# Kernel optimization log

Hardware: AMD Instinct MI355X
Metric: run time of the kernel (lower is better)

Reference implementation:

```python
import jax, jax.numpy as jnp
import numpy as np

K = 3          # kernel size
DIL = 1        # dilation
PAD = (K + (K - 1) * (DIL - 1)) // 2   # = 1
CENTER = (K * K - 1) // 2              # = 4
D_MIN = 0.0
D_MAX = 10.0
MIN_NGHBR = 4


def _unfold(x):
    """x: (B,C,H,W) -> patches (B,H,W,k*k,C), matching torch.nn.Unfold ordering."""
    b, c, h, w = x.shape
    xp = jnp.pad(x, ((0, 0), (0, 0), (PAD, PAD), (PAD, PAD)))
    # fixed k*k=9 taps: loop over the kernel window only (not data dims)
    pats = [xp[:, :, i * DIL:i * DIL + h, j * DIL:j * DIL + w]
            for i in range(K) for j in range(K)]
    p = jnp.stack(pats, axis=2)          # (B,C,kk,H,W)
    return p.transpose(0, 3, 4, 2, 1)    # (B,H,W,kk,C)


def setup_inputs() -> dict:
    key = jax.random.key(0)
    kxy, kz = jax.random.split(key)
    B, H, W = 4, 480, 640
    xy = jax.random.normal(kxy, (B, 2, H, W), dtype=jnp.float32)
    z = jax.random.uniform(kz, (B, 1, H, W), dtype=jnp.float32, minval=0.1, maxval=9.9)
    points = jnp.concatenate([xy, z], axis=1)  # (B,3,H,W)
    return {"points": points}


def reference(points):
    b, _, h, w = points.shape
    # 3x3 neighborhoods of 3D points: (B,H,W,9,3)
    A3 = _unfold(points)
    # depth-validity mask, unfolded over the same window: (B,H,W,9,1)
    depth = points[:, 2:3]
    valid = ((depth > D_MIN) & (depth < D_MAX)).astype(points.dtype)
    vc = _unfold(valid)
    # homogeneous design matrix A = [x y z 1], zeroed where neighbor invalid
    A = jnp.concatenate([A3, jnp.ones_like(A3[..., :1])], axis=-1)  # (B,H,W,9,4)
    A = jnp.where(vc > 0.5, A, jnp.zeros_like(A))
    # normal equations: per-pixel symmetric PSD 4x4
    AtA = jnp.einsum('bhwki,bhwkj->bhwij', A, A)
    # A^T A is symmetric PSD -> real eigensystem; eigh gives ascending eigvals,
    # so the null-space direction (smallest eigval) is column 0.
    eig_val, eig_vec = jnp.linalg.eigh(AtA)
    normal4 = eig_vec[..., :, 0]                      # (B,H,W,4)
    normal = normal4[..., :3].transpose(0, 3, 1, 2)   # (B,3,H,W)
    # F.normalize(p=2, dim=1, eps=1e-12)
    nrm = jnp.linalg.norm(normal, axis=1, keepdims=True)
    normal = normal / jnp.maximum(nrm, 1e-12)
    # orient toward the camera ray
    flip = jnp.sign(jnp.sum(normal * points, axis=1, keepdims=True))
    normal = normal * flip
    # validity masks
    vm1 = vc[:, :, :, CENTER, 0][:, None] > 0.5                 # center pixel valid
    vm2 = jnp.sum(vc[..., 0], axis=3)[:, None] >= MIN_NGHBR    # enough neighbors
    # vm3 (real eigensystem) is always True for the symmetric solve
    vm4 = jnp.linalg.norm(normal, axis=1, keepdims=True) > 0.5
    valid_mask = vm1 & vm2 & vm4
    return normal, valid_mask
```

## Files before the change

### kernel.cpp

```cpp
#include <hip/hip_runtime.h>

#define BB 4
#define HH 480
#define WW 640

__device__ __forceinline__ double det3d(double a, double b, double c,
                                        double d, double e, double f,
                                        double g, double h, double i) {
    return a * (e * i - f * h) - b * (d * i - f * g) + c * (d * h - e * g);
}

__global__ __launch_bounds__(256) void d2n_kernel(const float* __restrict__ pts,
                                                  float* __restrict__ out) {
    int idx = blockIdx.x * 256 + threadIdx.x;
    if (idx >= BB * HH * WW) return;
    int x = idx % WW;
    int t1 = idx / WW;
    int y = t1 % HH;
    int b = t1 / HH;

    const size_t HW = (size_t)HH * WW;
    const float* xs = pts + ((size_t)b * 3 + 0) * HW;
    const float* ys = pts + ((size_t)b * 3 + 1) * HW;
    const float* zs = pts + ((size_t)b * 3 + 2) * HW;

    float px[9], py[9], pz[9];
    bool inb[9];
#pragma unroll
    for (int i = 0; i < 9; ++i) {
        int dy = i / 3 - 1, dx = i % 3 - 1;
        int yy = y + dy, xx = x + dx;
        inb[i] = ((unsigned)yy < HH) & ((unsigned)xx < WW);
        int yyc = min(max(yy, 0), HH - 1);
        int xxc = min(max(xx, 0), WW - 1);
        int o = yyc * WW + xxc;
        pz[i] = zs[o];
        px[i] = xs[o];
        py[i] = ys[o];
    }

    float sxx = 0.f, sxy = 0.f, sxz = 0.f, sx = 0.f;
    float syy = 0.f, syz = 0.f, sy = 0.f;
    float szz = 0.f, sz = 0.f, cnt = 0.f;
#pragma unroll
    for (int i = 0; i < 9; ++i) {
        float w = (inb[i] && pz[i] > 0.0f && pz[i] < 10.0f) ? 1.0f : 0.0f;
        float qx = px[i] * w, qy = py[i] * w, qz = pz[i] * w;
        sxx += qx * px[i]; sxy += qx * py[i]; sxz += qx * pz[i]; sx += qx;
        syy += qy * py[i]; syz += qy * pz[i]; sy += qy;
        szz += qz * pz[i]; sz += qz;
        cnt += w;
    }

    double tr = (double)sxx + (double)syy + (double)szz + (double)cnt;
    double it = 1.0 / tr;
    double m00 = sxx * it, m01 = sxy * it, m02 = sxz * it, m03 = sx * it;
    double m11 = syy * it, m12 = syz * it, m13 = sy * it;
    double m22 = szz * it, m23 = sz * it, m33 = cnt * it;

    double e1 = m00 + m11 + m22 + m33;
    double e2 = (m00 * m11 - m01 * m01) + (m00 * m22 - m02 * m02) +
                (m00 * m33 - m03 * m03) + (m11 * m22 - m12 * m12) +
                (m11 * m33 - m13 * m13) + (m22 * m33 - m23 * m23);
    double P0 = det3d(m11, m12, m13, m12, m22, m23, m13, m23, m33);
    double P1 = det3d(m00, m02, m03, m02, m22, m23, m03, m23, m33);
    double P2 = det3d(m00, m01, m03, m01, m11, m13, m03, m13, m33);
    double P3 = det3d(m00, m01, m02, m01, m11, m12, m02, m12, m22);
    double e3 = P0 + P1 + P2 + P3;
    double e4 = m00 * P0
              - m01 * det3d(m01, m12, m13, m02, m22, m23, m03, m23, m33)
              + m02 * det3d(m01, m11, m13, m02, m12, m23, m03, m13, m33)
              - m03 * det3d(m01, m11, m12, m02, m12, m22, m03, m13, m23);

    double lam = 0.0;
#pragma unroll
    for (int itn = 0; itn < 16; ++itn) {
        double p  = (((lam - e1) * lam + e2) * lam - e3) * lam + e4;
        double dp = ((4.0 * lam - 3.0 * e1) * lam + 2.0 * e2) * lam - e3;
        dp = fmin(dp, -1e-300);
        lam = lam - p / dp;
        lam = fmin(fmax(lam, 0.0), 0.26);
    }

    double d0 = m00 - lam, d1 = m11 - lam, d2 = m22 - lam, d3 = m33 - lam;
    double C00 =  det3d(d1, m12, m13, m12, d2, m23, m13, m23, d3);
    double C01 = -det3d(m01, m12, m13, m02, d2, m23, m03, m23, d3);
    double C02 =  det3d(m01, d1, m13, m02, m12, m23, m03, m13, d3);
    double C03 = -det3d(m01, d1, m12, m02, m12, d2, m03, m13, m23);
    double C11 =  det3d(d0, m02, m03, m02, d2, m23, m03, m23, d3);
    double C12 = -det3d(d0, m01, m03, m02, m12, m23, m03, m13, d3);
    double C13 =  det3d(d0, m01, m02, m02, m12, d2, m03, m13, m23);
    double C22 =  det3d(d0, m01, m03, m01, d1, m13, m03, m13, d3);
    double C23 = -det3d(d0, m01, m02, m01, d1, m12, m03, m13, m23);
    double C33 =  det3d(d0, m01, m02, m01, d1, m12, m02, m12, d2);

    double best = fabs(C00);
    double vx = C00, vy = C01, vz = C02;
    double a1 = fabs(C11);
    if (a1 > best) { best = a1; vx = C01; vy = C11; vz = C12; }
    double a2 = fabs(C22);
    if (a2 > best) { best = a2; vx = C02; vy = C12; vz = C22; }
    double a3 = fabs(C33);
    if (a3 > best) { best = a3; vx = C03; vy = C13; vz = C23; }

    double nd = vx * vx + vy * vy + vz * vz;
    double inv = 1.0 / fmax(sqrt(nd), 1e-300);
    float nx = (float)(vx * inv), ny = (float)(vy * inv), nz = (float)(vz * inv);

    int o = y * WW + x;
    float cx = px[4], cy = py[4], cz = pz[4];
    float dot = nx * cx + ny * cy + nz * cz;
    float sgn = (dot > 0.0f) ? 1.0f : ((dot < 0.0f) ? -1.0f : 0.0f);
    nx *= sgn; ny *= sgn; nz *= sgn;

    out[((size_t)b * 3 + 0) * HW + o] = nx;
    out[((size_t)b * 3 + 1) * HW + o] = ny;
    out[((size_t)b * 3 + 2) * HW + o] = nz;

    bool cvalid = (cz > 0.0f && cz < 10.0f);
    bool m = cvalid && (cnt >= 4.0f) && (nx * nx + ny * ny + nz * nz > 0.25f);
    out[(size_t)BB * 3 * HW + (size_t)b * HW + o] = m ? 1.0f : 0.0f;
}

extern "C" void kernel_launch(void* const* d_in, const int* in_sizes, int n_in,
                              void* d_out, int out_size, void* d_ws, size_t ws_size,
                              hipStream_t stream) {
    const float* pts = (const float*)d_in[0];
    float* out = (float*)d_out;
    int total = BB * HH * WW;
    d2n_kernel<<<(total + 255) / 256, 256, 0, stream>>>(pts, out);
}
```

Before: 93.57 us.

## Cut fp64 cost: symmetric determinants, fast reciprocals, fewer Newton iterations

Replaces the fp64 divisions with a float hardware reciprocal refined by one Newton step, and uses a cheaper symmetric 3x3 determinant form for the principal minors and diagonal cofactors. It also trims the Newton eigenvalue iterations from 16 to 14, hoists the clamped row and column indices, and moves the final normalization to float using rsq after scaling by the chosen diagonal cofactor. The aim is to cut fp64 division and sqrt throughput costs, which dominate this compute-bound kernel. The risks are lower precision from the approximate reciprocal, fewer iterations, and overflow or zero handling in frcp(vd), all of which could change results in degenerate cases.

```diff
diff --git a/kernel.cpp b/kernel.cpp
--- a/kernel.cpp
+++ b/kernel.cpp
@@ -8,6 +8,18 @@
                                         double d, double e, double f,
                                         double g, double h, double i) {
     return a * (e * i - f * h) - b * (d * i - f * g) + c * (d * h - e * g);
+}
+
+__device__ __forceinline__ double sdet3d(double a, double b, double c,
+                                         double e, double f, double i) {
+    return a * (e * i - f * f) + b * (2.0 * c * f - b * i) - c * c * e;
+}
+
+__device__ __forceinline__ double frcp(double d) {
+    float rf = __builtin_amdgcn_rcpf((float)d);
+    double r = (double)rf;
+    r = r * __builtin_fma(-d, r, 2.0);
+    return r;
 }
 
 __global__ __launch_bounds__(256) void d2n_kernel(const float* __restrict__ pts,
@@ -24,16 +36,23 @@
     const float* ys = pts + ((size_t)b * 3 + 1) * HW;
     const float* zs = pts + ((size_t)b * 3 + 2) * HW;
 
+    int row[3], col[3];
+    bool rin[3], cin[3];
+#pragma unroll
+    for (int k = 0; k < 3; ++k) {
+        int yy = y + k - 1, xx = x + k - 1;
+        rin[k] = (unsigned)yy < HH;
+        cin[k] = (unsigned)xx < WW;
+        row[k] = min(max(yy, 0), HH - 1) * WW;
+        col[k] = min(max(xx, 0), WW - 1);
+    }
     float px[9], py[9], pz[9];
     bool inb[9];
 #pragma unroll
     for (int i = 0; i < 9; ++i) {
-        int dy = i / 3 - 1, dx = i % 3 - 1;
-        int yy = y + dy, xx = x + dx;
-        inb[i] = ((unsigned)yy < HH) & ((unsigned)xx < WW);
-        int yyc = min(max(yy, 0), HH - 1);
-        int xxc = min(max(xx, 0), WW - 1);
-        int o = yyc * WW + xxc;
+        int r = i / 3, c = i % 3;
+        int o = row[r] + col[c];
+        inb[i] = rin[r] & cin[c];
         pz[i] = zs[o];
         px[i] = xs[o];
         py[i] = ys[o];
@@ -53,7 +72,7 @@
     }
 
     double tr = (double)sxx + (double)syy + (double)szz + (double)cnt;
-    double it = 1.0 / tr;
+    double it = frcp(tr);
     double m00 = sxx * it, m01 = sxy * it, m02 = sxz * it, m03 = sx * it;
     double m11 = syy * it, m12 = syz * it, m13 = sy * it;
     double m22 = szz * it, m23 = sz * it, m33 = cnt * it;
@@ -62,50 +81,54 @@
     double e2 = (m00 * m11 - m01 * m01) + (m00 * m22 - m02 * m02) +
                 (m00 * m33 - m03 * m03) + (m11 * m22 - m12 * m12) +
                 (m11 * m33 - m13 * m13) + (m22 * m33 - m23 * m23);
-    double P0 = det3d(m11, m12, m13, m12, m22, m23, m13, m23, m33);
-    double P1 = det3d(m00, m02, m03, m02, m22, m23, m03, m23, m33);
-    double P2 = det3d(m00, m01, m03, m01, m11, m13, m03, m13, m33);
-    double P3 = det3d(m00, m01, m02, m01, m11, m12, m02, m12, m22);
+    double P0 = sdet3d(m11, m12, m13, m22, m23, m33);
+    double P1 = sdet3d(m00, m02, m03, m22, m23, m33);
+    double P2 = sdet3d(m00, m01, m03, m11, m13, m33);
+    double P3 = sdet3d(m00, m01, m02, m11, m12, m22);
     double e3 = P0 + P1 + P2 + P3;
     double e4 = m00 * P0
               - m01 * det3d(m01, m12, m13, m02, m22, m23, m03, m23, m33)
               + m02 * det3d(m01, m11, m13, m02, m12, m23, m03, m13, m33)
               - m03 * det3d(m01, m11, m12, m02, m12, m22, m03, m13, m23);
 
+    double t31 = 3.0 * e1, t22 = 2.0 * e2;
     double lam = 0.0;
 #pragma unroll
-    for (int itn = 0; itn < 16; ++itn) {
+    for (int itn = 0; itn < 14; ++itn) {
         double p  = (((lam - e1) * lam + e2) * lam - e3) * lam + e4;
-        double dp = ((4.0 * lam - 3.0 * e1) * lam + 2.0 * e2) * lam - e3;
-        dp = fmin(dp, -1e-300);
-        lam = lam - p / dp;
+        double dp = ((4.0 * lam - t31) * lam + t22) * lam - e3;
+        dp = fmin(dp, -1e-30);
+        lam = lam - p * frcp(dp);
         lam = fmin(fmax(lam, 0.0), 0.26);
     }
 
     double d0 = m00 - lam, d1 = m11 - lam, d2 = m22 - lam, d3 = m33 - lam;
-    double C00 =  det3d(d1, m12, m13, m12, d2, m23, m13, m23, d3);
+    double C00 =  sdet3d(d1, m12, m13, d2, m23, d3);
+    double C11 =  sdet3d(d0, m02, m03, d2, m23, d3);
+    double C22 =  sdet3d(d0, m01, m03, d1, m13, d3);
+    double C33 =  sdet3d(d0, m01, m02, d1, m12, d2);
     double C01 = -det3d(m01, m12, m13, m02, d2, m23, m03, m23, d3);
     double C02 =  det3d(m01, d1, m13, m02, m12, m23, m03, m13, d3);
     double C03 = -det3d(m01, d1, m12, m02, m12, d2, m03, m13, m23);
-    double C11 =  det3d(d0, m02, m03, m02, d2, m23, m03, m23, d3);
     double C12 = -det3d(d0, m01, m03, m02, m12, m23, m03, m13, d3);
     double C13 =  det3d(d0, m01, m02, m02, m12, d2, m03, m13, m23);
-    double C22 =  det3d(d0, m01, m03, m01, d1, m13, m03, m13, d3);
     double C23 = -det3d(d0, m01, m02, m01, d1, m12, m03, m13, m23);
-    double C33 =  det3d(d0, m01, m02, m01, d1, m12, m02, m12, d2);
 
     double best = fabs(C00);
-    double vx = C00, vy = C01, vz = C02;
+    double vx = C00, vy = C01, vz = C02, vd = C00;
     double a1 = fabs(C11);
-    if (a1 > best) { best = a1; vx = C01; vy = C11; vz = C12; }
+    if (a1 > best) { best = a1; vx = C01; vy = C11; vz = C12; vd = C11; }
     double a2 = fabs(C22);
-    if (a2 > best) { best = a2; vx = C02; vy = C12; vz = C22; }
+    if (a2 > best) { best = a2; vx = C02; vy = C12; vz = C22; vd = C22; }
     double a3 = fabs(C33);
-    if (a3 > best) { best = a3; vx = C03; vy = C13; vz = C23; }
+    if (a3 > best) { best = a3; vx = C03; vy = C13; vz = C23; vd = C33; }
 
-    double nd = vx * vx + vy * vy + vz * vz;
-    double inv = 1.0 / fmax(sqrt(nd), 1e-300);
-    float nx = (float)(vx * inv), ny = (float)(vy * inv), nz = (float)(vz * inv);
+    double sc = frcp(vd);
+    float fx = (float)(vx * sc), fy = (float)(vy * sc), fz = (float)(vz * sc);
+
+    float nd = fx * fx + fy * fy + fz * fz;
+    float inv = __builtin_amdgcn_rsqf(fmaxf(nd, 1e-30f));
+    float nx = fx * inv, ny = fy * inv, nz = fz * inv;
 
     int o = y * WW + x;
     float cx = px[4], cy = py[4], cz = pz[4];
```

New measurement: 87.94 us. -6.0%, faster.
